# Optimization experiments

Hardware: AMD Instinct MI355X
Metric: run time of the kernel (lower is better)

The kernel has to match this reference:

```python
import jax, jax.numpy as jnp
import numpy as np

B, L, D, H = 4, 2048, 1024, 16
HD = D // H  # head_dim = 64


def setup_inputs() -> dict:
    key = jax.random.key(0)
    ks = jax.random.split(key, 13)
    s = 1.0 / np.sqrt(D)
    inp = {
        'q': jax.random.normal(ks[0], (B, L, D), jnp.float32),
        'k': jax.random.normal(ks[1], (B, L, D), jnp.float32),
        'v': jax.random.normal(ks[2], (B, L, D), jnp.float32),
        'mask': jax.random.randint(ks[3], (B, 1, L, L), 0, 2, jnp.int32),
        'WQ': jax.random.normal(ks[4], (D, D), jnp.float32) * s,
        'bQ': jnp.zeros((D,), jnp.float32),
        'WK': jax.random.normal(ks[5], (D, D), jnp.float32) * s,
        'bK': jnp.zeros((D,), jnp.float32),
        'WV': jax.random.normal(ks[6], (D, D), jnp.float32) * s,
        'bV': jnp.zeros((D,), jnp.float32),
        'WO': jax.random.normal(ks[7], (D, D), jnp.float32) * s,
        'bO': jnp.zeros((D,), jnp.float32),
    }
    return inp


def reference(q, k, v, mask, WQ, bQ, WK, bK, WV, bV, WO, bO):
    # Linear projections (torch Linear: x @ W.T + b; here W stored as [D,D], use x @ W + b equivalently)
    Q = q @ WQ + bQ  # [B, L, D]
    K = k @ WK + bK
    V = v @ WV + bV
    # split heads -> [B, H, L, HD]
    Q = Q.reshape(B, L, H, HD).transpose(0, 2, 1, 3)
    K = K.reshape(B, L, H, HD).transpose(0, 2, 1, 3)
    V = V.reshape(B, L, H, HD).transpose(0, 2, 1, 3)
    scale = 1.0 / np.sqrt(HD).astype(np.float32)
    scores = jnp.einsum('bhqd,bhkd->bhqk', Q, K) * scale  # [B, H, Lq, Lk]
    scores = jnp.where(mask == 0, -jnp.inf, scores)  # mask broadcasts over heads
    attn = jax.nn.softmax(scores, axis=-1)
    # dropout p=0 (eval) -> identity
    ctx = jnp.einsum('bhqk,bhkd->bhqd', attn, V)  # [B, H, L, HD]
    ctx = ctx.transpose(0, 2, 1, 3).reshape(B, L, D)
    return ctx @ WO + bO
```

## Files before the change

kernel.cpp:

```cpp
#include <hip/hip_runtime.h>
#include <math.h>

#define B_  4
#define L_  2048
#define D_  1024
#define H_  16
#define HD_ 64

typedef __attribute__((ext_vector_type(8))) short short8;
typedef __attribute__((ext_vector_type(4))) float f32x4;

__device__ static inline unsigned short f2bf(float f) {
    union { float f; unsigned int u; } v; v.f = f;
    const unsigned int u = v.u;
    return (unsigned short)((u + 0x7FFFu + ((u >> 16) & 1u)) >> 16);
}

__device__ static inline unsigned cvt_pk_bf16(float a, float b) {
    unsigned r;
    asm("v_cvt_pk_bf16_f32 %0, %1, %2" : "=v"(r) : "v"(a), "v"(b));
    return r;
}

__device__ static inline void async_copy16(const void* g, void* lds)
{
    __builtin_amdgcn_global_load_lds(
        (const __attribute__((address_space(1))) void*)g,
        (__attribute__((address_space(3))) void*)lds, 16, 0, 0);
}

__global__ __launch_bounds__(256) void cvt3_bf16_kernel(
    const float* __restrict__ i0, const float* __restrict__ i1,
    const float* __restrict__ i2,
    unsigned short* __restrict__ o0, unsigned short* __restrict__ o1,
    unsigned short* __restrict__ o2)
{
    const float* in = blockIdx.y == 0 ? i0 : blockIdx.y == 1 ? i1 : i2;
    unsigned short* out = blockIdx.y == 0 ? o0 : blockIdx.y == 1 ? o1 : o2;
    const size_t i = ((size_t)blockIdx.x * 256 + threadIdx.x) * 8;
    const float4 x = *(const float4*)&in[i];
    const float4 y = *(const float4*)&in[i + 4];
    ushort4 a0, a1;
    a0.x = f2bf(x.x); a0.y = f2bf(x.y); a0.z = f2bf(x.z); a0.w = f2bf(x.w);
    a1.x = f2bf(y.x); a1.y = f2bf(y.y); a1.z = f2bf(y.z); a1.w = f2bf(y.w);
    *(ushort4*)&out[i]     = a0;
    *(ushort4*)&out[i + 4] = a1;
}

__global__ __launch_bounds__(256) void transpose_bf16_kernel(
    const float* __restrict__ W, unsigned short* __restrict__ WT)
{
    __shared__ float t[32][33];
    const int c  = threadIdx.x & 31;
    const int r8 = threadIdx.x >> 5;
    const int k0 = blockIdx.y * 32;
    const int n0 = blockIdx.x * 32;
    #pragma unroll
    for (int i = 0; i < 4; ++i) {
        const int r = r8 + i * 8;
        t[r][c] = W[(size_t)(k0 + r) * 1024 + n0 + c];
    }
    __syncthreads();
    #pragma unroll
    for (int i = 0; i < 4; ++i) {
        const int r = r8 + i * 8;
        WT[(size_t)(n0 + r) * 1024 + k0 + c] = f2bf(t[c][r]);
    }
}

__global__ __launch_bounds__(256) void trans3_bf16_kernel(
    const float* __restrict__ W0, const float* __restrict__ W1,
    const float* __restrict__ W2,
    unsigned short* __restrict__ T0, unsigned short* __restrict__ T1,
    unsigned short* __restrict__ T2)
{
    __shared__ float t[32][33];
    const float* W = blockIdx.z == 0 ? W0 : blockIdx.z == 1 ? W1 : W2;
    unsigned short* WT = blockIdx.z == 0 ? T0 : blockIdx.z == 1 ? T1 : T2;
    const int c  = threadIdx.x & 31;
    const int r8 = threadIdx.x >> 5;
    const int k0 = blockIdx.y * 32;
    const int n0 = blockIdx.x * 32;
    #pragma unroll
    for (int i = 0; i < 4; ++i) {
        const int r = r8 + i * 8;
        t[r][c] = W[(size_t)(k0 + r) * 1024 + n0 + c];
    }
    __syncthreads();
    #pragma unroll
    for (int i = 0; i < 4; ++i) {
        const int r = r8 + i * 8;
        WT[(size_t)(n0 + r) * 1024 + k0 + c] = f2bf(t[c][r]);
    }
}

__global__ __launch_bounds__(256) void vtrans_bf16_kernel(
    const unsigned short* __restrict__ Vb, unsigned short* __restrict__ vtb)
{
    __shared__ unsigned short t[64][68];
    const int tid = threadIdx.x;
    const int l0  = blockIdx.x * 64;
    const int h   = blockIdx.y;
    const int b   = blockIdx.z;
    const int rr  = tid >> 4;
    const int c4  = (tid & 15) * 4;
    #pragma unroll
    for (int i = 0; i < 4; ++i) {
        const int r = i * 16 + rr;
        *(ushort4*)&t[r][c4] =
            *(const ushort4*)&Vb[((size_t)(b * L_ + l0 + r)) * D_ + h * 64 + c4];
    }
    __syncthreads();
    #pragma unroll
    for (int i = 0; i < 4; ++i) {
        const int d = i * 16 + rr;
        ushort4 o;
        o.x = t[c4 + 0][d]; o.y = t[c4 + 1][d];
        o.z = t[c4 + 2][d]; o.w = t[c4 + 3][d];
        *(ushort4*)&vtb[((size_t)((b * H_ + h) * 64 + d)) * L_ + l0 + c4] = o;
    }
}

__global__ __launch_bounds__(256) void pack_mask16_kernel(
    const int* __restrict__ mask, unsigned short* __restrict__ mbt)
{
    const unsigned g = blockIdx.x * 256 + threadIdx.x;
    const int v = mask[g];
    const unsigned long long bm = __ballot(v != 0);
    const int lane = threadIdx.x & 63;
    if (lane < 4) {
        const int b  = g >> 22;
        const int q  = (g >> 11) & 2047;
        const int kt = (g >> 6) & 31;
        unsigned long long x = (bm >> (4 * lane)) & 0x000F000F000F000FULL;
        x |= x >> 12;
        x |= x >> 24;
        mbt[((size_t)(b * 32 + kt) * 2048 + q) * 4 + lane] =
            (unsigned short)(x & 0xFFFFu);
    }
}

template<int OUT_BF16>
__device__ static inline void gemm_body(
    const unsigned short* __restrict__ A, const unsigned short* __restrict__ WT,
    const float* __restrict__ bias, void* __restrict__ Cv,
    int M, int N, int K, float omul,
    unsigned short* At, unsigned short* Bt)
{
    const int tid  = threadIdx.x;
    const int lane = tid & 63;
    const int wave = tid >> 6;
    const int wm   = wave >> 1;
    const int wn   = wave & 1;
    const int quad = lane >> 4;
    const int l15  = lane & 15;
    const int m0   = blockIdx.y * 128;
    const int n0   = blockIdx.x * 128;

    f32x4 acc[4][4];
    #pragma unroll
    for (int i = 0; i < 4; ++i)
        #pragma unroll
        for (int j = 0; j < 4; ++j) acc[i][j] = (f32x4)0.f;

    for (int k0 = 0; k0 < K; k0 += 64) {
        __syncthreads();
        #pragma unroll
        for (int i = 0; i < 4; ++i) {
            const int fb  = i * 256 + wave * 64;
            const int f   = fb + lane;
            const int row = f >> 3;
            const int c8  = f & 7;
            async_copy16(&A [(size_t)(m0 + row) * K + k0 + c8 * 8],
                         (char*)At + (size_t)fb * 16);
            async_copy16(&WT[(size_t)(n0 + row) * K + k0 + c8 * 8],
                         (char*)Bt + (size_t)fb * 16);
        }
        __syncthreads();

        #pragma unroll
        for (int kk = 0; kk < 64; kk += 32) {
            short8 afr[4], bfr[4];
            #pragma unroll
            for (int mt = 0; mt < 4; ++mt)
                afr[mt] = *(const short8*)&At[(size_t)(wm * 64 + mt * 16 + l15) * 64 + kk + quad * 8];
            #pragma unroll
            for (int nt = 0; nt < 4; ++nt)
                bfr[nt] = *(const short8*)&Bt[(size_t)(wn * 64 + nt * 16 + l15) * 64 + kk + quad * 8];
            __builtin_amdgcn_s_setprio(1);
            #pragma unroll
            for (int mt = 0; mt < 4; ++mt)
                #pragma unroll
                for (int nt = 0; nt < 4; ++nt)
                    acc[mt][nt] = __builtin_amdgcn_mfma_f32_16x16x32_bf16(
                        afr[mt], bfr[nt], acc[mt][nt], 0, 0, 0);
            __builtin_amdgcn_s_setprio(0);
        }
    }

    #pragma unroll
    for (int nt = 0; nt < 4; ++nt) {
        const int col = n0 + wn * 64 + nt * 16 + l15;
        const float bv = bias[col];
        #pragma unroll
        for (int mt = 0; mt < 4; ++mt) {
            const int r0 = m0 + wm * 64 + mt * 16 + quad * 4;
            #pragma unroll
            for (int r = 0; r < 4; ++r) {
                const float val = (acc[mt][nt][r] + bv) * omul;
                if constexpr (OUT_BF16)
                    ((unsigned short*)Cv)[(size_t)(r0 + r) * N + col] = f2bf(val);
                else
                    ((float*)Cv)[(size_t)(r0 + r) * N + col] = val;
            }
        }
    }
}

__global__ __launch_bounds__(256) void gemm3_mfma_kernel(
    const unsigned short* __restrict__ A0, const unsigned short* __restrict__ A1,
    const unsigned short* __restrict__ A2,
    const unsigned short* __restrict__ W0, const unsigned short* __restrict__ W1,
    const unsigned short* __restrict__ W2,
    const float* __restrict__ b0, const float* __restrict__ b1,
    const float* __restrict__ b2,
    unsigned short* __restrict__ C0, unsigned short* __restrict__ C1,
    unsigned short* __restrict__ C2, float om0)
{
    __shared__ __align__(16) unsigned short At[128 * 64];
    __shared__ __align__(16) unsigned short Bt[128 * 64];
    const int z = blockIdx.z;
    const unsigned short* A  = z == 0 ? A0 : z == 1 ? A1 : A2;
    const unsigned short* WT = z == 0 ? W0 : z == 1 ? W1 : W2;
    const float* bias        = z == 0 ? b0 : z == 1 ? b1 : b2;
    unsigned short* C        = z == 0 ? C0 : z == 1 ? C1 : C2;
    const float omul         = z == 0 ? om0 : 1.f;
    gemm_body<1>(A, WT, bias, C, B_ * L_, D_, D_, omul, At, Bt);
}

__global__ __launch_bounds__(256) void gemm_mfma_kernel(
    const unsigned short* __restrict__ A, const unsigned short* __restrict__ WT,
    const float* __restrict__ bias, float* __restrict__ C,
    int M, int N, int K)
{
    __shared__ __align__(16) unsigned short At[128 * 64];
    __shared__ __align__(16) unsigned short Bt[128 * 64];
    gemm_body<0>(A, WT, bias, C, M, N, K, 1.f, At, Bt);
}

#define AQ 128
#define AK 64
#define PSTR 72
#define NT (L_ / AK)

__global__ __launch_bounds__(256) void attn_mfma_kernel(
    const unsigned short* __restrict__ Qb,
    const unsigned short* __restrict__ Kb,
    const unsigned short* __restrict__ Vtg,
    const unsigned short* __restrict__ mbt,
    unsigned short* __restrict__ Cb)
{
    __shared__ __align__(16) unsigned short Kt[2][AK * 64];
    __shared__ __align__(16) unsigned short Vs[2][64 * AK];
    __shared__ __align__(16) unsigned short Pt[AQ * PSTR];
    __shared__ __align__(16) unsigned short Mt[2][AQ * 4];

    const int tid  = threadIdx.x;
    const int lane = tid & 63;
    const int w    = tid >> 6;
    const int quad = lane >> 4;
    const int l15  = lane & 15;

    const int nid = (blockIdx.x & 7) * 128 + (blockIdx.x >> 3);
    const int q0  = (nid & 15) * AQ;
    const int h   = (nid >> 4) & 15;
    const int b   = nid >> 8;

    const unsigned short* kbase = &Kb [((size_t)(b * L_)) * D_ + h * 64];
    const unsigned short* vbase = &Vtg[((size_t)((b * H_ + h) * 64)) * L_];
    const unsigned short* mbase = &mbt[((size_t)(b * 32) * 2048 + q0) * 4];

    short8 qf[2][2];
    #pragma unroll
    for (int qc = 0; qc < 2; ++qc)
        #pragma unroll
        for (int kc = 0; kc < 2; ++kc)
            qf[qc][kc] = *(const short8*)
                &Qb[((size_t)(b * L_ + q0 + w * 32 + qc * 16 + l15)) * D_
                    + h * 64 + kc * 32 + quad * 8];

    f32x4 ot[4][2];
    #pragma unroll
    for (int dr = 0; dr < 4; ++dr)
        #pragma unroll
        for (int qc = 0; qc < 2; ++qc) ot[dr][qc] = (f32x4)0.f;
    float m_run[2] = {-INFINITY, -INFINITY};
    float l_run[2] = {0.f, 0.f};

    auto stage = [&](int bi, int kt) {
        const int k0 = kt * AK;
        #pragma unroll
        for (int i = 0; i < 2; ++i) {
            const int fb = i * 256 + w * 64;
            const int f  = fb + lane;
            const int r  = f >> 3;
            const int cs = (f & 7) ^ (r & 7);
            async_copy16(&kbase[(size_t)(k0 + r) * D_ + cs * 8],
                         (char*)&Kt[bi][0] + fb * 16);
            async_copy16(&vbase[(size_t)r * L_ + k0 + cs * 8],
                         (char*)&Vs[bi][0] + fb * 16);
        }
        if (w == 3)
            async_copy16(&mbase[(size_t)kt * 2048 * 4 + lane * 8],
                         (char*)&Mt[bi][0]);
    };

    stage(0, 0);
    __syncthreads();

    for (int kt = 0; kt < NT; ++kt) {
        const int cur = kt & 1;
        if (kt + 1 < NT) stage(cur ^ 1, kt + 1);

        f32x4 st[4][2];
        {
            short8 kf[4];
            #pragma unroll
            for (int kr = 0; kr < 4; ++kr)
                kf[kr] = *(const short8*)
                    &Kt[cur][(kr * 16 + l15) * 64 + ((quad ^ (l15 & 7)) * 8)];
            __builtin_amdgcn_s_setprio(1);
            #pragma unroll
            for (int kr = 0; kr < 4; ++kr)
                #pragma unroll
                for (int qc = 0; qc < 2; ++qc)
                    st[kr][qc] = __builtin_amdgcn_mfma_f32_16x16x32_bf16(
                        kf[kr], qf[qc][0], (f32x4)0.f, 0, 0, 0);
            __builtin_amdgcn_s_setprio(0);
        }
        {
            short8 kf[4];
            #pragma unroll
            for (int kr = 0; kr < 4; ++kr)
                kf[kr] = *(const short8*)
                    &Kt[cur][(kr * 16 + l15) * 64 + (((4 + quad) ^ (l15 & 7)) * 8)];
            __builtin_amdgcn_s_setprio(1);
            #pragma unroll
            for (int kr = 0; kr < 4; ++kr)
                #pragma unroll
                for (int qc = 0; qc < 2; ++qc)
                    st[kr][qc] = __builtin_amdgcn_mfma_f32_16x16x32_bf16(
                        kf[kr], qf[qc][1], st[kr][qc], 0, 0, 0);
            __builtin_amdgcn_s_setprio(0);
        }

        #pragma unroll
        for (int qc = 0; qc < 2; ++qc) {
            const unsigned m16 = Mt[cur][(w * 32 + qc * 16 + l15) * 4 + quad];
            float rmax = -INFINITY;
            #pragma unroll
            for (int kr = 0; kr < 4; ++kr) {
                const unsigned nib = (m16 >> (kr * 4)) & 0xFu;
                #pragma unroll
                for (int r = 0; r < 4; ++r) {
                    const float x = ((nib >> r) & 1u) ? st[kr][qc][r] : -INFINITY;
                    st[kr][qc][r] = x;
                    rmax = fmaxf(rmax, x);
                }
            }
            rmax = fmaxf(rmax, __shfl_xor(rmax, 16));
            rmax = fmaxf(rmax, __shfl_xor(rmax, 32));
            if (__any(rmax > m_run[qc] + 8.f)) {
                const float mnew  = fmaxf(m_run[qc], rmax);
                const float msafe = fmaxf(mnew, -1e30f);
                const float alpha = exp2f(m_run[qc] - msafe);
                l_run[qc] *= alpha;
                #pragma unroll
                for (int dr = 0; dr < 4; ++dr) {
                    ot[dr][qc][0] *= alpha; ot[dr][qc][1] *= alpha;
                    ot[dr][qc][2] *= alpha; ot[dr][qc][3] *= alpha;
                }
                m_run[qc] = mnew;
            }
            const float msafe = fmaxf(m_run[qc], -1e30f);
            float psum = 0.f;
            #pragma unroll
            for (int kr = 0; kr < 4; ++kr) {
                const float p0 = exp2f(st[kr][qc][0] - msafe);
                const float p1 = exp2f(st[kr][qc][1] - msafe);
                const float p2 = exp2f(st[kr][qc][2] - msafe);
                const float p3 = exp2f(st[kr][qc][3] - msafe);
                psum += (p0 + p1) + (p2 + p3);
                uint2 pk;
                pk.x = cvt_pk_bf16(p0, p1);
                pk.y = cvt_pk_bf16(p2, p3);
                *(uint2*)&Pt[(w * 32 + qc * 16 + l15) * PSTR + kr * 16 + quad * 4] = pk;
            }
            psum += __shfl_xor(psum, 16);
            psum += __shfl_xor(psum, 32);
            l_run[qc] += psum;
        }

        #pragma unroll
        for (int kc = 0; kc < 2; ++kc) {
            short8 vf[4], pf[2];
            #pragma unroll
            for (int dr = 0; dr < 4; ++dr)
                vf[dr] = *(const short8*)
                    &Vs[cur][(dr * 16 + l15) * 64 + (((kc * 4 + quad) ^ (l15 & 7)) * 8)];
            #pragma unroll
            for (int qc = 0; qc < 2; ++qc)
                pf[qc] = *(const short8*)&Pt[(w * 32 + qc * 16 + l15) * PSTR
                                             + kc * 32 + quad * 8];
            __builtin_amdgcn_s_setprio(1);
            #pragma unroll
            for (int dr = 0; dr < 4; ++dr)
                #pragma unroll
                for (int qc = 0; qc < 2; ++qc)
                    ot[dr][qc] = __builtin_amdgcn_mfma_f32_16x16x32_bf16(
                        vf[dr], pf[qc], ot[dr][qc], 0, 0, 0);
            __builtin_amdgcn_s_setprio(0);
        }

        __syncthreads();
    }

    #pragma unroll
    for (int qc = 0; qc < 2; ++qc) {
        const float rinv = (l_run[qc] > 0.f) ? (1.f / l_run[qc]) : 0.f;
        const size_t base = ((size_t)(b * L_ + q0 + w * 32 + qc * 16 + l15)) * D_
                            + h * 64;
        #pragma unroll
        for (int dr = 0; dr < 4; ++dr) {
            ushort4 o;
            o.x = f2bf(ot[dr][qc][0] * rinv);
            o.y = f2bf(ot[dr][qc][1] * rinv);
            o.z = f2bf(ot[dr][qc][2] * rinv);
            o.w = f2bf(ot[dr][qc][3] * rinv);
            *(ushort4*)&Cb[base + dr * 16 + quad * 4] = o;
        }
    }
}

extern "C" void kernel_launch(void* const* d_in, const int* in_sizes, int n_in,
                              void* d_out, int out_size, void* d_ws, size_t ws_size,
                              hipStream_t stream)
{
    const float* q    = (const float*)d_in[0];
    const float* k    = (const float*)d_in[1];
    const float* v    = (const float*)d_in[2];
    const int*   mask = (const int*)d_in[3];
    const float* WQ   = (const float*)d_in[4];
    const float* bQ   = (const float*)d_in[5];
    const float* WK   = (const float*)d_in[6];
    const float* bK   = (const float*)d_in[7];
    const float* WV   = (const float*)d_in[8];
    const float* bV   = (const float*)d_in[9];
    const float* WO   = (const float*)d_in[10];
    const float* bO   = (const float*)d_in[11];
    float* out = (float*)d_out;

    const size_t NTOK = (size_t)B_ * L_;

    char* W = (char*)d_ws;
    unsigned short* qin = (unsigned short*)(W);
    unsigned short* kin = (unsigned short*)(W + ((size_t)16  << 20));
    unsigned short* vin = (unsigned short*)(W + ((size_t)32  << 20));
    unsigned short* qbf = (unsigned short*)(W + ((size_t)48  << 20));
    unsigned short* kbf = (unsigned short*)(W + ((size_t)64  << 20));
    unsigned short* vbf = (unsigned short*)(W + ((size_t)80  << 20));
    unsigned short* vtb = (unsigned short*)(W + ((size_t)96  << 20));
    unsigned short* cb  = (unsigned short*)(W + ((size_t)112 << 20));
    unsigned short* WTo = vin;

    unsigned short* mbt16 = (unsigned short*)d_out;
    unsigned short* WTq = (unsigned short*)((char*)d_out + ((size_t)2 << 20));
    unsigned short* WTk = (unsigned short*)((char*)d_out + ((size_t)4 << 20));
    unsigned short* WTv = (unsigned short*)((char*)d_out + ((size_t)6 << 20));

    pack_mask16_kernel<<<(B_ * L_ * L_) / 256, 256, 0, stream>>>(mask, mbt16);

    const int cvtg = (int)(NTOK * D_ / (256 * 8));
    cvt3_bf16_kernel<<<dim3(cvtg, 3), 256, 0, stream>>>(q, k, v, qin, kin, vin);

    trans3_bf16_kernel<<<dim3(32, 32, 3), 256, 0, stream>>>(
        WQ, WK, WV, WTq, WTk, WTv);

    const float qscale = 0.125f * 1.44269504088896340736f;
    dim3 ggrd3(D_ / 128, NTOK / 128, 3);
    gemm3_mfma_kernel<<<ggrd3, 256, 0, stream>>>(
        qin, kin, vin, WTq, WTk, WTv, bQ, bK, bV, qbf, kbf, vbf, qscale);

    transpose_bf16_kernel<<<dim3(32, 32), 256, 0, stream>>>(WO, WTo);
    vtrans_bf16_kernel<<<dim3(L_ / 64, H_, B_), 256, 0, stream>>>(vbf, vtb);

    attn_mfma_kernel<<<dim3(1024), 256, 0, stream>>>(qbf, kbf, vtb, mbt16, cb);

    dim3 ggrd(D_ / 128, NTOK / 128);
    gemm_mfma_kernel<<<ggrd, 256, 0, stream>>>(cb, WTo, bO, out, (int)NTOK, D_, D_);
}
```

Before: 509.1 us.

## Single-buffer attention K/V tiles with register prefetch to raise occupancy

The attention kernel's double-buffered LDS tiles for K and V are replaced by single buffers. The next tile is prefetched into registers with global loads and written to LDS between two barriers at the end of each iteration. Launch bounds now request 4 blocks per CU. The aim is to cut LDS footprint and raise occupancy, at the cost of an extra barrier per iteration, more registers for staging, and exposed global-load latency where loads previously overlapped asynchronously.

Measured after the change: 623.2 us. +22.4%, slower.

```diff
diff --git a/kernel.cpp b/kernel.cpp
--- a/kernel.cpp
+++ b/kernel.cpp
@@ -253,15 +253,15 @@
 #define PSTR 72
 #define NT (L_ / AK)
 
-__global__ __launch_bounds__(256) void attn_mfma_kernel(
+__global__ __launch_bounds__(256, 4) void attn_mfma_kernel(
     const unsigned short* __restrict__ Qb,
     const unsigned short* __restrict__ Kb,
     const unsigned short* __restrict__ Vtg,
     const unsigned short* __restrict__ mbt,
     unsigned short* __restrict__ Cb)
 {
-    __shared__ __align__(16) unsigned short Kt[2][AK * 64];
-    __shared__ __align__(16) unsigned short Vs[2][64 * AK];
+    __shared__ __align__(16) unsigned short Kt[AK * 64];
+    __shared__ __align__(16) unsigned short Vs[64 * AK];
     __shared__ __align__(16) unsigned short Pt[AQ * PSTR];
     __shared__ __align__(16) unsigned short Mt[2][AQ * 4];
 
@@ -280,6 +280,15 @@
     const unsigned short* vbase = &Vtg[((size_t)((b * H_ + h) * 64)) * L_];
     const unsigned short* mbase = &mbt[((size_t)(b * 32) * 2048 + q0) * 4];
 
+    int srow[2], scol[2], sf[2];
+    #pragma unroll
+    for (int i = 0; i < 2; ++i) {
+        const int f = i * 256 + w * 64 + lane;
+        sf[i]   = f;
+        srow[i] = f >> 3;
+        scol[i] = ((f & 7) ^ ((f >> 3) & 7)) * 8;
+    }
+
     short8 qf[2][2];
     #pragma unroll
     for (int qc = 0; qc < 2; ++qc)
@@ -297,30 +306,32 @@
     float m_run[2] = {-INFINITY, -INFINITY};
     float l_run[2] = {0.f, 0.f};
 
-    auto stage = [&](int bi, int kt) {
-        const int k0 = kt * AK;
-        #pragma unroll
-        for (int i = 0; i < 2; ++i) {
-            const int fb = i * 256 + w * 64;
-            const int f  = fb + lane;
-            const int r  = f >> 3;
-            const int cs = (f & 7) ^ (r & 7);
-            async_copy16(&kbase[(size_t)(k0 + r) * D_ + cs * 8],
-                         (char*)&Kt[bi][0] + fb * 16);
-            async_copy16(&vbase[(size_t)r * L_ + k0 + cs * 8],
-                         (char*)&Vs[bi][0] + fb * 16);
-        }
-        if (w == 3)
-            async_copy16(&mbase[(size_t)kt * 2048 * 4 + lane * 8],
-                         (char*)&Mt[bi][0]);
-    };
-
-    stage(0, 0);
+    #pragma unroll
+    for (int i = 0; i < 2; ++i) {
+        async_copy16(&kbase[(size_t)srow[i] * D_ + scol[i]],
+                     (char*)Kt + sf[i] / 64 * 1024 + (sf[i] & 63) * 16);
+        async_copy16(&vbase[(size_t)srow[i] * L_ + scol[i]],
+                     (char*)Vs + sf[i] / 64 * 1024 + (sf[i] & 63) * 16);
+    }
+    if (w == 3)
+        async_copy16(&mbase[lane * 8], (char*)&Mt[0][0]);
     __syncthreads();
 
     for (int kt = 0; kt < NT; ++kt) {
         const int cur = kt & 1;
-        if (kt + 1 < NT) stage(cur ^ 1, kt + 1);
+
+        short8 kstg[2], vstg[2];
+        if (kt + 1 < NT) {
+            const int k1 = (kt + 1) * AK;
+            #pragma unroll
+            for (int i = 0; i < 2; ++i) {
+                kstg[i] = *(const short8*)&kbase[(size_t)(k1 + srow[i]) * D_ + scol[i]];
+                vstg[i] = *(const short8*)&vbase[(size_t)srow[i] * L_ + k1 + scol[i]];
+            }
+            if (w == 3)
+                async_copy16(&mbase[(size_t)(kt + 1) * 2048 * 4 + lane * 8],
+                             (char*)&Mt[cur ^ 1][0]);
+        }
 
         f32x4 st[4][2];
         {
@@ -328,7 +339,7 @@
             #pragma unroll
             for (int kr = 0; kr < 4; ++kr)
                 kf[kr] = *(const short8*)
-                    &Kt[cur][(kr * 16 + l15) * 64 + ((quad ^ (l15 & 7)) * 8)];
+                    &Kt[(kr * 16 + l15) * 64 + ((quad ^ (l15 & 7)) * 8)];
             __builtin_amdgcn_s_setprio(1);
             #pragma unroll
             for (int kr = 0; kr < 4; ++kr)
@@ -343,7 +354,7 @@
             #pragma unroll
             for (int kr = 0; kr < 4; ++kr)
                 kf[kr] = *(const short8*)
-                    &Kt[cur][(kr * 16 + l15) * 64 + (((4 + quad) ^ (l15 & 7)) * 8)];
+                    &Kt[(kr * 16 + l15) * 64 + (((4 + quad) ^ (l15 & 7)) * 8)];
             __builtin_amdgcn_s_setprio(1);
             #pragma unroll
             for (int kr = 0; kr < 4; ++kr)
@@ -407,7 +418,7 @@
             #pragma unroll
             for (int dr = 0; dr < 4; ++dr)
                 vf[dr] = *(const short8*)
-                    &Vs[cur][(dr * 16 + l15) * 64 + (((kc * 4 + quad) ^ (l15 & 7)) * 8)];
+                    &Vs[(dr * 16 + l15) * 64 + (((kc * 4 + quad) ^ (l15 & 7)) * 8)];
             #pragma unroll
             for (int qc = 0; qc < 2; ++qc)
                 pf[qc] = *(const short8*)&Pt[(w * 32 + qc * 16 + l15) * PSTR
@@ -422,7 +433,15 @@
             __builtin_amdgcn_s_setprio(0);
         }
 
-        __syncthreads();
+        if (kt + 1 < NT) {
+            __syncthreads();
+            #pragma unroll
+            for (int i = 0; i < 2; ++i) {
+                *(short8*)((char*)Kt + sf[i] * 16) = kstg[i];
+                *(short8*)((char*)Vs + sf[i] * 16) = vstg[i];
+            }
+            __syncthreads();
+        }
     }
 
     #pragma unroll
```

## Keep softmax probabilities in registers via cross-lane shuffles instead of LDS

Applied to the files above, without the earlier changes.

The P tile is no longer staged through shared memory. Each lane keeps its packed bf16 probabilities in registers, and the B-operand fragments for the PV MFMA are rebuilt with __shfl permutes plus selects. This drops an LDS write/read round trip and frees about 18KB of LDS per block, and launch bounds now request 4 blocks per CU for higher occupancy. In exchange it issues 16 bpermute shuffles per PV chunk and adds register pressure under the tighter occupancy bound.

Result: no change. 500.2 us (-1.7%).

```diff
diff --git a/kernel.cpp b/kernel.cpp
--- a/kernel.cpp
+++ b/kernel.cpp
@@ -9,6 +9,7 @@
 
 typedef __attribute__((ext_vector_type(8))) short short8;
 typedef __attribute__((ext_vector_type(4))) float f32x4;
+typedef __attribute__((ext_vector_type(4))) int   i32x4;
 
 __device__ static inline unsigned short f2bf(float f) {
     union { float f; unsigned int u; } v; v.f = f;
@@ -250,10 +251,9 @@
 
 #define AQ 128
 #define AK 64
-#define PSTR 72
 #define NT (L_ / AK)
 
-__global__ __launch_bounds__(256) void attn_mfma_kernel(
+__global__ __launch_bounds__(256, 4) void attn_mfma_kernel(
     const unsigned short* __restrict__ Qb,
     const unsigned short* __restrict__ Kb,
     const unsigned short* __restrict__ Vtg,
@@ -262,7 +262,6 @@
 {
     __shared__ __align__(16) unsigned short Kt[2][AK * 64];
     __shared__ __align__(16) unsigned short Vs[2][64 * AK];
-    __shared__ __align__(16) unsigned short Pt[AQ * PSTR];
     __shared__ __align__(16) unsigned short Mt[2][AQ * 4];
 
     const int tid  = threadIdx.x;
@@ -318,6 +317,10 @@
     stage(0, 0);
     __syncthreads();
 
+    const int srcA = ((quad & 1) << 5) + l15;
+    const int srcB = srcA + 16;
+    const bool selHi = (quad & 2) != 0;
+
     for (int kt = 0; kt < NT; ++kt) {
         const int cur = kt & 1;
         if (kt + 1 < NT) stage(cur ^ 1, kt + 1);
@@ -354,6 +357,7 @@
             __builtin_amdgcn_s_setprio(0);
         }
 
+        uint2 pk[2][4];
         #pragma unroll
         for (int qc = 0; qc < 2; ++qc) {
             const unsigned m16 = Mt[cur][(w * 32 + qc * 16 + l15) * 4 + quad];
@@ -391,10 +395,8 @@
                 const float p2 = exp2f(st[kr][qc][2] - msafe);
                 const float p3 = exp2f(st[kr][qc][3] - msafe);
                 psum += (p0 + p1) + (p2 + p3);
-                uint2 pk;
-                pk.x = cvt_pk_bf16(p0, p1);
-                pk.y = cvt_pk_bf16(p2, p3);
-                *(uint2*)&Pt[(w * 32 + qc * 16 + l15) * PSTR + kr * 16 + quad * 4] = pk;
+                pk[qc][kr].x = cvt_pk_bf16(p0, p1);
+                pk[qc][kr].y = cvt_pk_bf16(p2, p3);
             }
             psum += __shfl_xor(psum, 16);
             psum += __shfl_xor(psum, 32);
@@ -409,9 +411,24 @@
                 vf[dr] = *(const short8*)
                     &Vs[cur][(dr * 16 + l15) * 64 + (((kc * 4 + quad) ^ (l15 & 7)) * 8)];
             #pragma unroll
-            for (int qc = 0; qc < 2; ++qc)
-                pf[qc] = *(const short8*)&Pt[(w * 32 + qc * 16 + l15) * PSTR
-                                             + kc * 32 + quad * 8];
+            for (int qc = 0; qc < 2; ++qc) {
+                const uint2 lo = pk[qc][kc * 2];
+                const uint2 hi = pk[qc][kc * 2 + 1];
+                const int ax = __shfl((int)lo.x, srcA, 64);
+                const int ay = __shfl((int)lo.y, srcA, 64);
+                const int az = __shfl((int)lo.x, srcB, 64);
+                const int aw = __shfl((int)lo.y, srcB, 64);
+                const int bx = __shfl((int)hi.x, srcA, 64);
+                const int by = __shfl((int)hi.y, srcA, 64);
+                const int bz = __shfl((int)hi.x, srcB, 64);
+                const int bw = __shfl((int)hi.y, srcB, 64);
+                i32x4 t;
+                t.x = selHi ? bx : ax;
+                t.y = selHi ? by : ay;
+                t.z = selHi ? bz : az;
+                t.w = selHi ? bw : aw;
+                pf[qc] = *reinterpret_cast<short8*>(&t);
+            }
             __builtin_amdgcn_s_setprio(1);
             #pragma unroll
             for (int dr = 0; dr < 4; ++dr)
```

## Switch attention to 32x32x16 MFMA and pass P through registers instead of LDS

Applied to the files above, without the earlier changes.

The attention kernel now uses 32x32x16 bf16 MFMA tiles, so each lane owns a single query row. The softmax probabilities are repacked with cross-half lane shuffles into the B operand for the PV product, which removes the LDS P buffer and its writes and reads. The mask packing changes to 32-bit words to match the new lane layout, and launch bounds now request 4 blocks per CU. The per-row reductions need fewer shuffles, but more registers are live per lane, which could limit occupancy.

Measured after the change: 480.2 us. -5.7%, faster.

```diff
diff --git a/kernel.cpp b/kernel.cpp
--- a/kernel.cpp
+++ b/kernel.cpp
@@ -9,6 +9,8 @@
 
 typedef __attribute__((ext_vector_type(8))) short short8;
 typedef __attribute__((ext_vector_type(4))) float f32x4;
+typedef __attribute__((ext_vector_type(16))) float f32x16;
+typedef __attribute__((ext_vector_type(4))) int   i32x4;
 
 __device__ static inline unsigned short f2bf(float f) {
     union { float f; unsigned int u; } v; v.f = f;
@@ -121,23 +123,19 @@
     }
 }
 
-__global__ __launch_bounds__(256) void pack_mask16_kernel(
-    const int* __restrict__ mask, unsigned short* __restrict__ mbt)
+__global__ __launch_bounds__(256) void pack_mask32_kernel(
+    const int* __restrict__ mask, unsigned int* __restrict__ mm)
 {
     const unsigned g = blockIdx.x * 256 + threadIdx.x;
     const int v = mask[g];
     const unsigned long long bm = __ballot(v != 0);
     const int lane = threadIdx.x & 63;
-    if (lane < 4) {
-        const int b  = g >> 22;
-        const int q  = (g >> 11) & 2047;
-        const int kt = (g >> 6) & 31;
-        unsigned long long x = (bm >> (4 * lane)) & 0x000F000F000F000FULL;
-        x |= x >> 12;
-        x |= x >> 24;
-        mbt[((size_t)(b * 32 + kt) * 2048 + q) * 4 + lane] =
-            (unsigned short)(x & 0xFFFFu);
-    }
+    const int b = g >> 22;
+    const int q = (g >> 11) & 2047;
+    const int k = g & 2047;
+    const unsigned idx = ((unsigned)(b * 32 + (k >> 6)) * 2048 + q) * 2 + ((k >> 5) & 1);
+    if (lane == 0)       mm[idx] = (unsigned)bm;
+    else if (lane == 32) mm[idx] = (unsigned)(bm >> 32);
 }
 
 template<int OUT_BF16>
@@ -250,26 +248,24 @@
 
 #define AQ 128
 #define AK 64
-#define PSTR 72
 #define NT (L_ / AK)
 
-__global__ __launch_bounds__(256) void attn_mfma_kernel(
+__global__ __launch_bounds__(256, 4) void attn_mfma_kernel(
     const unsigned short* __restrict__ Qb,
     const unsigned short* __restrict__ Kb,
     const unsigned short* __restrict__ Vtg,
-    const unsigned short* __restrict__ mbt,
+    const unsigned int* __restrict__ mbt,
     unsigned short* __restrict__ Cb)
 {
     __shared__ __align__(16) unsigned short Kt[2][AK * 64];
     __shared__ __align__(16) unsigned short Vs[2][64 * AK];
-    __shared__ __align__(16) unsigned short Pt[AQ * PSTR];
-    __shared__ __align__(16) unsigned short Mt[2][AQ * 4];
+    __shared__ __align__(16) unsigned int   Mt[2][AQ * 2];
 
     const int tid  = threadIdx.x;
     const int lane = tid & 63;
     const int w    = tid >> 6;
-    const int quad = lane >> 4;
-    const int l15  = lane & 15;
+    const int hi   = lane >> 5;
+    const int l31  = lane & 31;
 
     const int nid = (blockIdx.x & 7) * 128 + (blockIdx.x >> 3);
     const int q0  = (nid & 15) * AQ;
@@ -278,24 +274,21 @@
 
     const unsigned short* kbase = &Kb [((size_t)(b * L_)) * D_ + h * 64];
     const unsigned short* vbase = &Vtg[((size_t)((b * H_ + h) * 64)) * L_];
-    const unsigned short* mbase = &mbt[((size_t)(b * 32) * 2048 + q0) * 4];
-
-    short8 qf[2][2];
-    #pragma unroll
-    for (int qc = 0; qc < 2; ++qc)
-        #pragma unroll
-        for (int kc = 0; kc < 2; ++kc)
-            qf[qc][kc] = *(const short8*)
-                &Qb[((size_t)(b * L_ + q0 + w * 32 + qc * 16 + l15)) * D_
-                    + h * 64 + kc * 32 + quad * 8];
-
-    f32x4 ot[4][2];
-    #pragma unroll
-    for (int dr = 0; dr < 4; ++dr)
-        #pragma unroll
-        for (int qc = 0; qc < 2; ++qc) ot[dr][qc] = (f32x4)0.f;
-    float m_run[2] = {-INFINITY, -INFINITY};
-    float l_run[2] = {0.f, 0.f};
+    const unsigned int*   mbase = &mbt[((size_t)(b * 32) * 2048 + q0) * 2];
+
+    const int q = q0 + w * 32 + l31;
+
+    short8 qf[4];
+    #pragma unroll
+    for (int ds = 0; ds < 4; ++ds)
+        qf[ds] = *(const short8*)
+            &Qb[((size_t)(b * L_ + q)) * D_ + h * 64 + ds * 16 + hi * 8];
+
+    f32x16 ot[2];
+    ot[0] = (f32x16)0.f; ot[1] = (f32x16)0.f;
+    float m_run = -INFINITY, l_run = 0.f;
+
+    const int swz = l31 & 7;
 
     auto stage = [&](int bi, int kt) {
         const int k0 = kt * AK;
@@ -311,7 +304,7 @@
                          (char*)&Vs[bi][0] + fb * 16);
         }
         if (w == 3)
-            async_copy16(&mbase[(size_t)kt * 2048 * 4 + lane * 8],
+            async_copy16(&mbase[(size_t)kt * 2048 * 2 + lane * 4],
                          (char*)&Mt[bi][0]);
     };
 
@@ -322,124 +315,129 @@
         const int cur = kt & 1;
         if (kt + 1 < NT) stage(cur ^ 1, kt + 1);
 
-        f32x4 st[4][2];
+        f32x16 st0, st1;
         {
-            short8 kf[4];
-            #pragma unroll
-            for (int kr = 0; kr < 4; ++kr)
-                kf[kr] = *(const short8*)
-                    &Kt[cur][(kr * 16 + l15) * 64 + ((quad ^ (l15 & 7)) * 8)];
+            short8 kf0 = *(const short8*)
+                &Kt[cur][(l31) * 64 + ((0 * 2 + hi) ^ swz) * 8];
+            short8 kf1 = *(const short8*)
+                &Kt[cur][(32 + l31) * 64 + ((0 * 2 + hi) ^ swz) * 8];
             __builtin_amdgcn_s_setprio(1);
-            #pragma unroll
-            for (int kr = 0; kr < 4; ++kr)
-                #pragma unroll
-                for (int qc = 0; qc < 2; ++qc)
-                    st[kr][qc] = __builtin_amdgcn_mfma_f32_16x16x32_bf16(
-                        kf[kr], qf[qc][0], (f32x4)0.f, 0, 0, 0);
+            st0 = __builtin_amdgcn_mfma_f32_32x32x16_bf16(
+                kf0, qf[0], (f32x16)0.f, 0, 0, 0);
+            st1 = __builtin_amdgcn_mfma_f32_32x32x16_bf16(
+                kf1, qf[0], (f32x16)0.f, 0, 0, 0);
             __builtin_amdgcn_s_setprio(0);
         }
-        {
-            short8 kf[4];
-            #pragma unroll
-            for (int kr = 0; kr < 4; ++kr)
-                kf[kr] = *(const short8*)
-                    &Kt[cur][(kr * 16 + l15) * 64 + (((4 + quad) ^ (l15 & 7)) * 8)];
+        #pragma unroll
+        for (int ds = 1; ds < 4; ++ds) {
+            short8 kf0 = *(const short8*)
+                &Kt[cur][(l31) * 64 + ((ds * 2 + hi) ^ swz) * 8];
+            short8 kf1 = *(const short8*)
+                &Kt[cur][(32 + l31) * 64 + ((ds * 2 + hi) ^ swz) * 8];
             __builtin_amdgcn_s_setprio(1);
-            #pragma unroll
-            for (int kr = 0; kr < 4; ++kr)
-                #pragma unroll
-                for (int qc = 0; qc < 2; ++qc)
-                    st[kr][qc] = __builtin_amdgcn_mfma_f32_16x16x32_bf16(
-                        kf[kr], qf[qc][1], st[kr][qc], 0, 0, 0);
+            st0 = __builtin_amdgcn_mfma_f32_32x32x16_bf16(
+                kf0, qf[ds], st0, 0, 0, 0);
+            st1 = __builtin_amdgcn_mfma_f32_32x32x16_bf16(
+                kf1, qf[ds], st1, 0, 0, 0);
             __builtin_amdgcn_s_setprio(0);
         }
 
-        #pragma unroll
-        for (int qc = 0; qc < 2; ++qc) {
-            const unsigned m16 = Mt[cur][(w * 32 + qc * 16 + l15) * 4 + quad];
-            float rmax = -INFINITY;
-            #pragma unroll
-            for (int kr = 0; kr < 4; ++kr) {
-                const unsigned nib = (m16 >> (kr * 4)) & 0xFu;
+        const uint2 mm = *(const uint2*)&Mt[cur][(w * 32 + l31) * 2];
+        float rmax = -INFINITY;
+        #pragma unroll
+        for (int kr = 0; kr < 2; ++kr) {
+            const unsigned w32 = kr ? mm.y : mm.x;
+            #pragma unroll
+            for (int s = 0; s < 4; ++s) {
+                const unsigned nib = (w32 >> (s * 8 + hi * 4)) & 0xFu;
                 #pragma unroll
                 for (int r = 0; r < 4; ++r) {
-                    const float x = ((nib >> r) & 1u) ? st[kr][qc][r] : -INFINITY;
-                    st[kr][qc][r] = x;
+                    float x = kr ? st1[s * 4 + r] : st0[s * 4 + r];
+                    x = ((nib >> r) & 1u) ? x : -INFINITY;
+                    if (kr) st1[s * 4 + r] = x; else st0[s * 4 + r] = x;
                     rmax = fmaxf(rmax, x);
                 }
             }
-            rmax = fmaxf(rmax, __shfl_xor(rmax, 16));
-            rmax = fmaxf(rmax, __shfl_xor(rmax, 32));
-            if (__any(rmax > m_run[qc] + 8.f)) {
-                const float mnew  = fmaxf(m_run[qc], rmax);
-                const float msafe = fmaxf(mnew, -1e30f);
-                const float alpha = exp2f(m_run[qc] - msafe);
-                l_run[qc] *= alpha;
+        }
+        rmax = fmaxf(rmax, __shfl_xor(rmax, 32));
+        if (__any(rmax > m_run + 8.f)) {
+            const float mnew  = fmaxf(m_run, rmax);
+            const float alpha = __builtin_amdgcn_exp2f(
+                m_run - fmaxf(mnew, -1e30f));
+            l_run *= alpha;
+            #pragma unroll
+            for (int db = 0; db < 2; ++db)
                 #pragma unroll
-                for (int dr = 0; dr < 4; ++dr) {
-                    ot[dr][qc][0] *= alpha; ot[dr][qc][1] *= alpha;
-                    ot[dr][qc][2] *= alpha; ot[dr][qc][3] *= alpha;
-                }
-                m_run[qc] = mnew;
+                for (int i = 0; i < 16; ++i) ot[db][i] *= alpha;
+            m_run = mnew;
+        }
+        const float msafe = fmaxf(m_run, -1e30f);
+        float psum = 0.f;
+        #pragma unroll
+        for (int kr = 0; kr < 2; ++kr)
+            #pragma unroll
+            for (int i = 0; i < 16; ++i) {
+                const float p = __builtin_amdgcn_exp2f(
+                    (kr ? st1[i] : st0[i]) - msafe);
+                if (kr) st1[i] = p; else st0[i] = p;
+                psum += p;
             }
-            const float msafe = fmaxf(m_run[qc], -1e30f);
-            float psum = 0.f;
-            #pragma unroll
-            for (int kr = 0; kr < 4; ++kr) {
-                const float p0 = exp2f(st[kr][qc][0] - msafe);
-                const float p1 = exp2f(st[kr][qc][1] - msafe);
-                const float p2 = exp2f(st[kr][qc][2] - msafe);
-                const float p3 = exp2f(st[kr][qc][3] - msafe);
-                psum += (p0 + p1) + (p2 + p3);
-                uint2 pk;
-                pk.x = cvt_pk_bf16(p0, p1);
-                pk.y = cvt_pk_bf16(p2, p3);
-                *(uint2*)&Pt[(w * 32 + qc * 16 + l15) * PSTR + kr * 16 + quad * 4] = pk;
+        psum += __shfl_xor(psum, 32);
+        l_run += psum;
+
+        #pragma unroll
+        for (int ks = 0; ks < 4; ++ks) {
+            const int sA = (ks & 1) * 2;
+            short8 vf0 = *(const short8*)
+                &Vs[cur][(l31) * 64 + ((ks * 2 + hi) ^ swz) * 8];
+            short8 vf1 = *(const short8*)
+                &Vs[cur][(32 + l31) * 64 + ((ks * 2 + hi) ^ swz) * 8];
+            unsigned cLo0, cLo1, cHi0, cHi1;
+            if (ks >> 1) {
+                cLo0 = cvt_pk_bf16(st1[sA*4+0], st1[sA*4+1]);
+                cLo1 = cvt_pk_bf16(st1[sA*4+2], st1[sA*4+3]);
+                cHi0 = cvt_pk_bf16(st1[sA*4+4], st1[sA*4+5]);
+                cHi1 = cvt_pk_bf16(st1[sA*4+6], st1[sA*4+7]);
+            } else {
+                cLo0 = cvt_pk_bf16(st0[sA*4+0], st0[sA*4+1]);
+                cLo1 = cvt_pk_bf16(st0[sA*4+2], st0[sA*4+3]);
+                cHi0 = cvt_pk_bf16(st0[sA*4+4], st0[sA*4+5]);
+                cHi1 = cvt_pk_bf16(st0[sA*4+6], st0[sA*4+7]);
             }
-            psum += __shfl_xor(psum, 16);
-            psum += __shfl_xor(psum, 32);
-            l_run[qc] += psum;
-        }
-
-        #pragma unroll
-        for (int kc = 0; kc < 2; ++kc) {
-            short8 vf[4], pf[2];
-            #pragma unroll
-            for (int dr = 0; dr < 4; ++dr)
-                vf[dr] = *(const short8*)
-                    &Vs[cur][(dr * 16 + l15) * 64 + (((kc * 4 + quad) ^ (l15 & 7)) * 8)];
-            #pragma unroll
-            for (int qc = 0; qc < 2; ++qc)
-                pf[qc] = *(const short8*)&Pt[(w * 32 + qc * 16 + l15) * PSTR
-                                             + kc * 32 + quad * 8];
+            const int xLo0 = __shfl_xor((int)cLo0, 32);
+            const int xLo1 = __shfl_xor((int)cLo1, 32);
+            const int xHi0 = __shfl_xor((int)cHi0, 32);
+            const int xHi1 = __shfl_xor((int)cHi1, 32);
+            i32x4 t;
+            t.x = hi ? xHi0 : (int)cLo0;
+            t.y = hi ? xHi1 : (int)cLo1;
+            t.z = hi ? (int)cHi0 : xLo0;
+            t.w = hi ? (int)cHi1 : xLo1;
+            const short8 pf = *reinterpret_cast<short8*>(&t);
             __builtin_amdgcn_s_setprio(1);
-            #pragma unroll
-            for (int dr = 0; dr < 4; ++dr)
-                #pragma unroll
-                for (int qc = 0; qc < 2; ++qc)
-                    ot[dr][qc] = __builtin_amdgcn_mfma_f32_16x16x32_bf16(
-                        vf[dr], pf[qc], ot[dr][qc], 0, 0, 0);
+            ot[0] = __builtin_amdgcn_mfma_f32_32x32x16_bf16(
+                vf0, pf, ot[0], 0, 0, 0);
+            ot[1] = __builtin_amdgcn_mfma_f32_32x32x16_bf16(
+                vf1, pf, ot[1], 0, 0, 0);
             __builtin_amdgcn_s_setprio(0);
         }
 
         __syncthreads();
     }
 
-    #pragma unroll
-    for (int qc = 0; qc < 2; ++qc) {
-        const float rinv = (l_run[qc] > 0.f) ? (1.f / l_run[qc]) : 0.f;
-        const size_t base = ((size_t)(b * L_ + q0 + w * 32 + qc * 16 + l15)) * D_
-                            + h * 64;
-        #pragma unroll
-        for (int dr = 0; dr < 4; ++dr) {
+    const float rinv = (l_run > 0.f) ? (1.f / l_run) : 0.f;
+    const size_t base = ((size_t)(b * L_ + q)) * D_ + h * 64;
+    #pragma unroll
+    for (int db = 0; db < 2; ++db)
+        #pragma unroll
+        for (int s = 0; s < 4; ++s) {
             ushort4 o;
-            o.x = f2bf(ot[dr][qc][0] * rinv);
-            o.y = f2bf(ot[dr][qc][1] * rinv);
-            o.z = f2bf(ot[dr][qc][2] * rinv);
-            o.w = f2bf(ot[dr][qc][3] * rinv);
-            *(ushort4*)&Cb[base + dr * 16 + quad * 4] = o;
-        }
-    }
+            o.x = f2bf(ot[db][s * 4 + 0] * rinv);
+            o.y = f2bf(ot[db][s * 4 + 1] * rinv);
+            o.z = f2bf(ot[db][s * 4 + 2] * rinv);
+            o.w = f2bf(ot[db][s * 4 + 3] * rinv);
+            *(ushort4*)&Cb[base + db * 32 + s * 8 + hi * 4] = o;
+        }
 }
 
 extern "C" void kernel_launch(void* const* d_in, const int* in_sizes, int n_in,
@@ -473,12 +471,12 @@
     unsigned short* cb  = (unsigned short*)(W + ((size_t)112 << 20));
     unsigned short* WTo = vin;
 
-    unsigned short* mbt16 = (unsigned short*)d_out;
+    unsigned int*   mbt32 = (unsigned int*)d_out;
     unsigned short* WTq = (unsigned short*)((char*)d_out + ((size_t)2 << 20));
     unsigned short* WTk = (unsigned short*)((char*)d_out + ((size_t)4 << 20));
     unsigned short* WTv = (unsigned short*)((char*)d_out + ((size_t)6 << 20));
 
-    pack_mask16_kernel<<<(B_ * L_ * L_) / 256, 256, 0, stream>>>(mask, mbt16);
+    pack_mask32_kernel<<<(B_ * L_ * L_) / 256, 256, 0, stream>>>(mask, mbt32);
 
     const int cvtg = (int)(NTOK * D_ / (256 * 8));
     cvt3_bf16_kernel<<<dim3(cvtg, 3), 256, 0, stream>>>(q, k, v, qin, kin, vin);
@@ -494,7 +492,7 @@
     transpose_bf16_kernel<<<dim3(32, 32), 256, 0, stream>>>(WO, WTo);
     vtrans_bf16_kernel<<<dim3(L_ / 64, H_, B_), 256, 0, stream>>>(vbf, vtb);
 
-    attn_mfma_kernel<<<dim3(1024), 256, 0, stream>>>(qbf, kbf, vtb, mbt16, cb);
+    attn_mfma_kernel<<<dim3(1024), 256, 0, stream>>>(qbf, kbf, vtb, mbt32, cb);
 
     dim3 ggrd(D_ / 128, NTOK / 128);
     gemm_mfma_kernel<<<ggrd, 256, 0, stream>>>(cb, WTo, bO, out, (int)NTOK, D_, D_);
```
